# Kernel tuning notes

Measured on AMD Instinct MI355X. Metric: run time of the kernel, lower is better.

Reference implementation:

```python
import jax, jax.numpy as jnp
import numpy as np

N_NODES = 100000
N_EDGES = 1600000
D_H = 64
D_E = 64
D_Q = 64
D_HID = 128
N_GRAPHS = 16


def _mlp_params(key, d_in, d_hid):
    k1, k2, k3, k4 = jax.random.split(key, 4)
    s1 = 1.0 / np.sqrt(d_in)
    s2 = 1.0 / np.sqrt(d_hid)
    return (
        jax.random.uniform(k1, (d_in, d_hid), jnp.float32, -s1, s1),
        jax.random.uniform(k2, (d_hid,), jnp.float32, -s1, s1),
        jax.random.uniform(k3, (d_hid, 1), jnp.float32, -s2, s2),
        jax.random.uniform(k4, (1,), jnp.float32, -s2, s2),
    )


def setup_inputs() -> dict:
    key = jax.random.key(0)
    ks = jax.random.split(key, 8)
    h = jax.random.normal(ks[0], (N_NODES, D_H), jnp.float32)
    e = jax.random.normal(ks[1], (N_EDGES, D_E), jnp.float32)
    q = jax.random.normal(ks[2], (N_GRAPHS, D_Q), jnp.float32)
    edge_index = jax.random.randint(ks[3], (2, N_EDGES), 0, N_NODES, jnp.int64)
    edge_batch = jax.random.randint(ks[4], (N_EDGES,), 0, N_GRAPHS, jnp.int64)
    gw1, gb1, gw2, gb2 = _mlp_params(ks[5], 2 * D_H + D_Q, D_HID)
    sw1, sb1, sw2, sb2 = _mlp_params(ks[6], 2 * D_H + D_E, D_HID)
    return {
        "h": h, "e": e, "q": q,
        "edge_index": edge_index, "edge_batch": edge_batch,
        "gate_w1": gw1, "gate_b1": gb1, "gate_w2": gw2, "gate_b2": gb2,
        "score_w1": sw1, "score_b1": sb1, "score_w2": sw2, "score_b2": sb2,
    }


def _mlp(x, w1, b1, w2, b2):
    # 2-layer MLP, no layernorm (use_layer_norm=False), output dim 1
    hidden = jax.nn.relu(x @ w1 + b1)
    return (hidden @ w2 + b2)[..., 0]


def _dst_softmax(raw, dst, num_nodes):
    # numerically stable per-destination softmax via segment reductions
    max_vals = jax.ops.segment_max(raw, dst, num_segments=num_nodes)
    exp_vals = jnp.exp(raw - max_vals[dst])
    sum_exp = jax.ops.segment_sum(exp_vals, dst, num_segments=num_nodes)
    denom = jnp.maximum(sum_exp[dst], 1e-9)
    return exp_vals / denom


def reference(h, e, q, edge_index, edge_batch,
              gate_w1, gate_b1, gate_w2, gate_b2,
              score_w1, score_b1, score_w2, score_b2):
    src, dst = edge_index[0], edge_index[1]
    h_i = h[src]            # [E, d_h]
    h_j = h[dst]            # [E, d_h]
    q_e = q[edge_batch]     # [E, d_q]
    gate_in = jnp.concatenate([h_i, h_j, q_e], axis=-1)
    gate = jax.nn.sigmoid(_mlp(gate_in, gate_w1, gate_b1, gate_w2, gate_b2))
    score_in = jnp.concatenate([h_i, h_j, e], axis=-1)
    score = _mlp(score_in, score_w1, score_b1, score_w2, score_b2)
    raw = gate * score
    return _dst_softmax(raw, dst, h.shape[0])
```

## Files before the change

kernel.cpp:

```cpp
#include <hip/hip_runtime.h>
#include <hip/hip_bf16.h>

#define NN 100000
#define NE 1600000

typedef __attribute__((ext_vector_type(8))) unsigned short ushort8v;
typedef __attribute__((ext_vector_type(8))) short short8v;
typedef __attribute__((ext_vector_type(4))) float f32x4;

__device__ __forceinline__ float b2f(unsigned short u) {
  return __uint_as_float(((unsigned)u) << 16);
}
__device__ __forceinline__ short f2bs(float f) {
  unsigned u = __float_as_uint(f);
  unsigned r = (u + 0x7FFFu + ((u >> 16) & 1u)) >> 16;
  return (short)r;
}

__global__ void qproj_kernel(const float* __restrict__ q,
                             const float* __restrict__ gw1,
                             const float* __restrict__ gb1,
                             float* __restrict__ Qg) {
  int g = blockIdx.x, j = threadIdx.x;
  float acc = gb1[j];
  for (int k = 0; k < 64; ++k) acc += q[g * 64 + k] * gw1[(128 + k) * 128 + j];
  Qg[g * 128 + j] = acc;
}

__global__ __launch_bounds__(1024) void prepack_kernel(
    const float* __restrict__ sw1, short8v* __restrict__ WtG) {
  int tid = threadIdx.x;
  int t = tid >> 7, ks = (tid >> 6) & 1, lane = tid & 63;
  int qg = lane >> 4, cl = lane & 15;
  int d = 32 * (cl >> 2) + 4 * t + (cl & 3);
  short8v fr;
#pragma unroll
  for (int j = 0; j < 8; ++j)
    fr[j] = f2bs(sw1[(128 + ks * 32 + qg * 8 + j) * 128 + d]);
  WtG[tid] = fr;
}

__global__ __launch_bounds__(256) void nodeproj_kernel(
    const float* __restrict__ h, const float* __restrict__ gw1,
    const float* __restrict__ sw1, __hip_bfloat16* __restrict__ SRCP,
    __hip_bfloat16* __restrict__ DSTP) {
  __shared__ float hs[64][64];
  __shared__ float Ws[64][128];
  int part = blockIdx.y;
  const float* W = (part & 1) ? sw1 : gw1;
  int roff = (part >= 2) ? 64 : 0;
  __hip_bfloat16* outp = (part >= 2) ? DSTP : SRCP;
  int goff = (part & 1) ? 32 : 0;
  int n0 = blockIdx.x * 64;
  int t = threadIdx.x;

  {
    int n = t & 63, kc = t >> 6;
    int gn = n0 + n;
#pragma unroll
    for (int i = 0; i < 4; ++i) {
      int k = kc * 16 + i * 4;
      float4 hv = make_float4(0.f, 0.f, 0.f, 0.f);
      if (gn < NN) hv = *(const float4*)&h[gn * 64 + k];
      hs[k + 0][n] = hv.x; hs[k + 1][n] = hv.y;
      hs[k + 2][n] = hv.z; hs[k + 3][n] = hv.w;
    }
  }
  {
    const float* Wb = W + roff * 128;
    float* wsf = &Ws[0][0];
#pragma unroll
    for (int i = 0; i < 8; ++i) {
      int flat = (i * 256 + t) * 4;
      *(float4*)&wsf[flat] = *(const float4*)&Wb[flat];
    }
  }
  __syncthreads();

  int tx = t & 31, ty = t >> 5;
  float acc[8][4] = {};
#pragma unroll 4
  for (int k = 0; k < 64; ++k) {
    float hn[8];
    *(float4*)&hn[0] = *(const float4*)&hs[k][ty * 8];
    *(float4*)&hn[4] = *(const float4*)&hs[k][ty * 8 + 4];
    float wv[4];
#pragma unroll
    for (int i = 0; i < 4; ++i) wv[i] = Ws[k][tx + 32 * i];
#pragma unroll
    for (int j = 0; j < 8; ++j)
#pragma unroll
      for (int i = 0; i < 4; ++i) acc[j][i] += hn[j] * wv[i];
  }
#pragma unroll
  for (int j = 0; j < 8; ++j) {
    int gn = n0 + ty * 8 + j;
    if (gn < NN) {
#pragma unroll
      for (int i = 0; i < 4; ++i)
        outp[(size_t)gn * 256 + i * 64 + goff + tx] = __float2bfloat16(acc[j][i]);
    }
  }
}

__global__ __launch_bounds__(256) void edge_kernel(
    const float* __restrict__ e, const int* __restrict__ eidx,
    const int* __restrict__ ebat,
    const __hip_bfloat16* __restrict__ SRCP, const __hip_bfloat16* __restrict__ DSTP,
    const float* __restrict__ Qg, const short8v* __restrict__ WtG,
    const float* __restrict__ sb1, const float* __restrict__ gw2,
    const float* __restrict__ gb2, const float* __restrict__ sw2,
    const float* __restrict__ sb2, float* __restrict__ out,
    float* __restrict__ nsum) {
  __shared__ short8v WtS[1024];
  __shared__ f32x4 QgS[16 * 33];
  __shared__ f32x4 gw2S[32], sb1S[32], sw2S[32];
  const int tid = threadIdx.x;
  const int w = tid >> 6, lane = tid & 63;
  const int qg = lane >> 4, cl = lane & 15;
  const int EB = blockIdx.x * 256 + w * 64;
  const unsigned short* SU = (const unsigned short*)SRCP;
  const unsigned short* DU = (const unsigned short*)DSTP;
  const float sb2v = sb2[0], gb2v = gb2[0];

  int srcv = eidx[EB + cl];
  int dstv = eidx[NE + EB + cl];
  int gv   = ebat[EB + cl];

  {
    const f32x4* s4 = (const f32x4*)WtG;
    f32x4* d4 = (f32x4*)WtS;
#pragma unroll
    for (int i = 0; i < 4; ++i) d4[tid + i * 256] = s4[tid + i * 256];
    const f32x4* q4 = (const f32x4*)Qg;
    QgS[(tid >> 5) * 33 + (tid & 31)] = q4[tid];
    {
      int t2 = tid + 256;
      QgS[(t2 >> 5) * 33 + (t2 & 31)] = q4[t2];
    }
    if (tid < 32) {
      gw2S[tid] = ((const f32x4*)gw2)[tid];
      sb1S[tid] = ((const f32x4*)sb1)[tid];
      sw2S[tid] = ((const f32x4*)sw2)[tid];
    }
  }
  __syncthreads();

#pragma unroll 1
  for (int rt = 0; rt < 4; ++rt) {
    const int erow = EB + rt * 16 + cl;

    const float* ap = e + (size_t)erow * 64 + qg * 8;
    f32x4 f0 = __builtin_nontemporal_load((const f32x4*)(ap + 0));
    f32x4 f1 = __builtin_nontemporal_load((const f32x4*)(ap + 4));
    f32x4 f2 = __builtin_nontemporal_load((const f32x4*)(ap + 32));
    f32x4 f3 = __builtin_nontemporal_load((const f32x4*)(ap + 36));

    const ushort8v* sp = (const ushort8v*)(SU + (size_t)srcv * 256 + qg * 64);
    const ushort8v* dp = (const ushort8v*)(DU + (size_t)dstv * 256 + qg * 64);
    ushort8v gav[4], gbv[4], sav[4], sbv[4];
#pragma unroll
    for (int c = 0; c < 4; ++c) {
      gav[c] = sp[c];
      gbv[c] = dp[c];
      sav[c] = sp[4 + c];
      sbv[c] = dp[4 + c];
    }

    int srcn = srcv, dstn = dstv, gn = gv;
    if (rt < 3) {
      int er2 = erow + 16;
      srcn = eidx[er2];
      dstn = eidx[NE + er2];
      gn   = ebat[er2];
    }

    short8v b0, b1;
    b0[0] = f2bs(f0.x); b0[1] = f2bs(f0.y); b0[2] = f2bs(f0.z); b0[3] = f2bs(f0.w);
    b0[4] = f2bs(f1.x); b0[5] = f2bs(f1.y); b0[6] = f2bs(f1.z); b0[7] = f2bs(f1.w);
    b1[0] = f2bs(f2.x); b1[1] = f2bs(f2.y); b1[2] = f2bs(f2.z); b1[3] = f2bs(f2.w);
    b1[4] = f2bs(f3.x); b1[5] = f2bs(f3.y); b1[6] = f2bs(f3.z); b1[7] = f2bs(f3.w);

    float gpart = 0.f;
#pragma unroll
    for (int c = 0; c < 4; ++c) {
      ushort8v av = gav[c], bv = gbv[c];
      f32x4 q0 = QgS[gv * 33 + qg * 8 + c * 2];
      f32x4 q1 = QgS[gv * 33 + qg * 8 + c * 2 + 1];
      f32x4 w0 = gw2S[qg * 8 + c * 2];
      f32x4 w1 = gw2S[qg * 8 + c * 2 + 1];
#pragma unroll
      for (int ii = 0; ii < 4; ++ii) {
        float x = b2f(av[ii]) + b2f(bv[ii]) + q0[ii];
        gpart = fmaf(fmaxf(x, 0.f), w0[ii], gpart);
      }
#pragma unroll
      for (int ii = 0; ii < 4; ++ii) {
        float x = b2f(av[4 + ii]) + b2f(bv[4 + ii]) + q1[ii];
        gpart = fmaf(fmaxf(x, 0.f), w1[ii], gpart);
      }
    }

    float part = 0.f;
#pragma unroll
    for (int t = 0; t < 8; ++t) {
      short8v Aw0 = WtS[(t * 2 + 0) * 64 + lane];
      short8v Aw1 = WtS[(t * 2 + 1) * 64 + lane];
      f32x4 acc = (f32x4){0.f, 0.f, 0.f, 0.f};
      acc = __builtin_amdgcn_mfma_f32_16x16x32_bf16(Aw0, b0, acc, 0, 0, 0);
      acc = __builtin_amdgcn_mfma_f32_16x16x32_bf16(Aw1, b1, acc, 0, 0, 0);
      f32x4 bb = sb1S[qg * 8 + t];
      f32x4 ww = sw2S[qg * 8 + t];
#pragma unroll
      for (int i = 0; i < 4; ++i) {
        float sx = acc[i] + b2f(sav[t >> 1][(t & 1) * 4 + i]) +
                   b2f(sbv[t >> 1][(t & 1) * 4 + i]) + bb[i];
        part = fmaf(fmaxf(sx, 0.f), ww[i], part);
      }
    }

    part += __shfl_xor(part, 16, 64);
    part += __shfl_xor(part, 32, 64);
    gpart += __shfl_xor(gpart, 16, 64);
    gpart += __shfl_xor(gpart, 32, 64);
    if (lane < 16) {
      int E = EB + rt * 16 + cl;
      float gate = 1.f / (1.f + __expf(-(gpart + gb2v)));
      float ex = __expf(gate * (part + sb2v));
      out[E] = ex;
      atomicAdd(&nsum[dstv], ex);
    }
    srcv = srcn; dstv = dstn; gv = gn;
  }
}

__global__ __launch_bounds__(256) void norm_kernel(
    const int* __restrict__ eidx, const float* __restrict__ nodesum,
    float* __restrict__ out) {
  int ee = blockIdx.x * 256 + threadIdx.x;
  int dst = eidx[NE + ee];
  out[ee] = out[ee] / fmaxf(nodesum[dst], 1e-9f);
}

extern "C" void kernel_launch(void* const* d_in, const int* in_sizes, int n_in,
                              void* d_out, int out_size, void* d_ws, size_t ws_size,
                              hipStream_t stream) {
  const float* h   = (const float*)d_in[0];
  const float* e   = (const float*)d_in[1];
  const float* q   = (const float*)d_in[2];
  const int* eidx  = (const int*)d_in[3];
  const int* ebat  = (const int*)d_in[4];
  const float* gw1 = (const float*)d_in[5];
  const float* gb1 = (const float*)d_in[6];
  const float* gw2 = (const float*)d_in[7];
  const float* gb2 = (const float*)d_in[8];
  const float* sw1 = (const float*)d_in[9];
  const float* sb1 = (const float*)d_in[10];
  const float* sw2 = (const float*)d_in[11];
  const float* sb2 = (const float*)d_in[12];
  float* out = (float*)d_out;

  char* ws = (char*)d_ws;
  __hip_bfloat16* SRCP = (__hip_bfloat16*)ws;
  __hip_bfloat16* DSTP = (__hip_bfloat16*)(ws + 51200000);
  float* Qg    = (float*)(ws + 102400000);
  short8v* WtG = (short8v*)(ws + 102400000 + 8192);
  float* nsum  = (float*)(ws + 102400000 + 8192 + 16384);

  (void)hipMemsetAsync(nsum, 0, 400000, stream);
  qproj_kernel<<<dim3(16), dim3(128), 0, stream>>>(q, gw1, gb1, Qg);
  prepack_kernel<<<dim3(1), dim3(1024), 0, stream>>>(sw1, WtG);
  nodeproj_kernel<<<dim3(1563, 4), dim3(256), 0, stream>>>(h, gw1, sw1, SRCP, DSTP);
  edge_kernel<<<dim3(NE / 256), dim3(256), 0, stream>>>(
      e, eidx, ebat, SRCP, DSTP, Qg, WtG, sb1, gw2, gb2, sw2, sb2, out, nsum);
  norm_kernel<<<dim3(NE / 256), dim3(256), 0, stream>>>(eidx, nsum, out);
}
```

Before: 547.4 us.

## Double-buffer edge gathers in edge_kernel and preload all edge indices

Replaces the serial per-row-tile loop in the edge kernel with a fully unrolled two-buffer software pipeline. The e-row loads and bf16 node-projection gathers for the next 16-edge tile are issued before the current tile is computed. All src/dst/batch indices for the wavefront's 64 edges are loaded up front, and launch bounds request two blocks per SM. This aims to hide gather latency behind MFMA work, at the cost of many more live registers, which could force spills or lower occupancy.

```diff
diff --git a/kernel.cpp b/kernel.cpp
--- a/kernel.cpp
+++ b/kernel.cpp
@@ -103,7 +103,7 @@
   }
 }
 
-__global__ __launch_bounds__(256) void edge_kernel(
+__global__ __launch_bounds__(256, 2) void edge_kernel(
     const float* __restrict__ e, const int* __restrict__ eidx,
     const int* __restrict__ ebat,
     const __hip_bfloat16* __restrict__ SRCP, const __hip_bfloat16* __restrict__ DSTP,
@@ -123,9 +123,12 @@
   const unsigned short* DU = (const unsigned short*)DSTP;
   const float sb2v = sb2[0], gb2v = gb2[0];
 
-  int srcv = eidx[EB + cl];
-  int dstv = eidx[NE + EB + cl];
-  int gv   = ebat[EB + cl];
+  const int src0 = eidx[EB + cl],      src1 = eidx[EB + 16 + cl];
+  const int src2 = eidx[EB + 32 + cl], src3 = eidx[EB + 48 + cl];
+  const int dst0 = eidx[NE + EB + cl],      dst1 = eidx[NE + EB + 16 + cl];
+  const int dst2 = eidx[NE + EB + 32 + cl], dst3 = eidx[NE + EB + 48 + cl];
+  const int g0 = ebat[EB + cl],      g1 = ebat[EB + 16 + cl];
+  const int g2 = ebat[EB + 32 + cl], g3 = ebat[EB + 48 + cl];
 
   {
     const f32x4* s4 = (const f32x4*)WtG;
@@ -146,45 +149,39 @@
   }
   __syncthreads();
 
-#pragma unroll 1
-  for (int rt = 0; rt < 4; ++rt) {
-    const int erow = EB + rt * 16 + cl;
-
-    const float* ap = e + (size_t)erow * 64 + qg * 8;
-    f32x4 f0 = __builtin_nontemporal_load((const f32x4*)(ap + 0));
-    f32x4 f1 = __builtin_nontemporal_load((const f32x4*)(ap + 4));
-    f32x4 f2 = __builtin_nontemporal_load((const f32x4*)(ap + 32));
-    f32x4 f3 = __builtin_nontemporal_load((const f32x4*)(ap + 36));
-
+  struct Buf {
+    f32x4 f[4];
+    ushort8v s[8];
+    ushort8v d[8];
+  };
+  Buf A, B;
+
+  auto stage = [&](Buf& S, int erow0, int srcv, int dstv) {
+    const float* ap = e + (size_t)(erow0 + cl) * 64 + qg * 8;
+    S.f[0] = __builtin_nontemporal_load((const f32x4*)(ap + 0));
+    S.f[1] = __builtin_nontemporal_load((const f32x4*)(ap + 4));
+    S.f[2] = __builtin_nontemporal_load((const f32x4*)(ap + 32));
+    S.f[3] = __builtin_nontemporal_load((const f32x4*)(ap + 36));
     const ushort8v* sp = (const ushort8v*)(SU + (size_t)srcv * 256 + qg * 64);
     const ushort8v* dp = (const ushort8v*)(DU + (size_t)dstv * 256 + qg * 64);
-    ushort8v gav[4], gbv[4], sav[4], sbv[4];
+#pragma unroll
+    for (int c = 0; c < 8; ++c) {
+      S.s[c] = sp[c];
+      S.d[c] = dp[c];
+    }
+  };
+
+  auto compute = [&](Buf& S, int erow0, int dstv, int gv) {
+    short8v b0, b1;
+    b0[0] = f2bs(S.f[0].x); b0[1] = f2bs(S.f[0].y); b0[2] = f2bs(S.f[0].z); b0[3] = f2bs(S.f[0].w);
+    b0[4] = f2bs(S.f[1].x); b0[5] = f2bs(S.f[1].y); b0[6] = f2bs(S.f[1].z); b0[7] = f2bs(S.f[1].w);
+    b1[0] = f2bs(S.f[2].x); b1[1] = f2bs(S.f[2].y); b1[2] = f2bs(S.f[2].z); b1[3] = f2bs(S.f[2].w);
+    b1[4] = f2bs(S.f[3].x); b1[5] = f2bs(S.f[3].y); b1[6] = f2bs(S.f[3].z); b1[7] = f2bs(S.f[3].w);
+
+    float gpart = 0.f;
 #pragma unroll
     for (int c = 0; c < 4; ++c) {
-      gav[c] = sp[c];
-      gbv[c] = dp[c];
-      sav[c] = sp[4 + c];
-      sbv[c] = dp[4 + c];
-    }
-
-    int srcn = srcv, dstn = dstv, gn = gv;
-    if (rt < 3) {
-      int er2 = erow + 16;
-      srcn = eidx[er2];
-      dstn = eidx[NE + er2];
-      gn   = ebat[er2];
-    }
-
-    short8v b0, b1;
-    b0[0] = f2bs(f0.x); b0[1] = f2bs(f0.y); b0[2] = f2bs(f0.z); b0[3] = f2bs(f0.w);
-    b0[4] = f2bs(f1.x); b0[5] = f2bs(f1.y); b0[6] = f2bs(f1.z); b0[7] = f2bs(f1.w);
-    b1[0] = f2bs(f2.x); b1[1] = f2bs(f2.y); b1[2] = f2bs(f2.z); b1[3] = f2bs(f2.w);
-    b1[4] = f2bs(f3.x); b1[5] = f2bs(f3.y); b1[6] = f2bs(f3.z); b1[7] = f2bs(f3.w);
-
-    float gpart = 0.f;
-#pragma unroll
-    for (int c = 0; c < 4; ++c) {
-      ushort8v av = gav[c], bv = gbv[c];
+      ushort8v av = S.s[c], bv = S.d[c];
       f32x4 q0 = QgS[gv * 33 + qg * 8 + c * 2];
       f32x4 q1 = QgS[gv * 33 + qg * 8 + c * 2 + 1];
       f32x4 w0 = gw2S[qg * 8 + c * 2];
@@ -213,8 +210,8 @@
       f32x4 ww = sw2S[qg * 8 + t];
 #pragma unroll
       for (int i = 0; i < 4; ++i) {
-        float sx = acc[i] + b2f(sav[t >> 1][(t & 1) * 4 + i]) +
-                   b2f(sbv[t >> 1][(t & 1) * 4 + i]) + bb[i];
+        float sx = acc[i] + b2f(S.s[4 + (t >> 1)][(t & 1) * 4 + i]) +
+                   b2f(S.d[4 + (t >> 1)][(t & 1) * 4 + i]) + bb[i];
         part = fmaf(fmaxf(sx, 0.f), ww[i], part);
       }
     }
@@ -224,14 +221,22 @@
     gpart += __shfl_xor(gpart, 16, 64);
     gpart += __shfl_xor(gpart, 32, 64);
     if (lane < 16) {
-      int E = EB + rt * 16 + cl;
+      int E = erow0 + cl;
       float gate = 1.f / (1.f + __expf(-(gpart + gb2v)));
       float ex = __expf(gate * (part + sb2v));
       out[E] = ex;
       atomicAdd(&nsum[dstv], ex);
     }
-    srcv = srcn; dstv = dstn; gv = gn;
-  }
+  };
+
+  stage(A, EB, src0, dst0);
+  stage(B, EB + 16, src1, dst1);
+  compute(A, EB, dst0, g0);
+  stage(A, EB + 32, src2, dst2);
+  compute(B, EB + 16, dst1, g1);
+  stage(B, EB + 48, src3, dst3);
+  compute(A, EB + 32, dst2, g2);
+  compute(B, EB + 48, dst3, g3);
 }
 
 __global__ __launch_bounds__(256) void norm_kernel(
```

Result: faster. 529.5 us (-3.3%).
